# Kernel optimization log

Hardware: AMD Instinct MI355X
Metric: run time of the kernel (lower is better)

Reference implementation:

```python
import jax, jax.numpy as jnp
import numpy as np

N_NODES = 50000
N_EDGES = 800000
IN_FEATS = 128
HIDDEN = 128
NUM_CLASSES = 47


def setup_inputs() -> dict:
    key = jax.random.key(0)
    k1, k2, k3, k4 = jax.random.split(key, 4)
    features = jax.random.normal(k1, (N_NODES, IN_FEATS), dtype=jnp.float32)
    edge_index = jax.random.randint(k2, (2, N_EDGES), 0, N_NODES, dtype=jnp.int32)
    # Glorot-style init for weights, zeros for bias (DGL GraphConv defaults)
    W1 = jax.random.normal(k3, (IN_FEATS, HIDDEN), dtype=jnp.float32) * (1.0 / np.sqrt(IN_FEATS))
    b1 = jnp.zeros((HIDDEN,), dtype=jnp.float32)
    W2 = jax.random.normal(k4, (HIDDEN, NUM_CLASSES), dtype=jnp.float32) * (1.0 / np.sqrt(HIDDEN))
    b2 = jnp.zeros((NUM_CLASSES,), dtype=jnp.float32)
    return {"features": features, "edge_index": edge_index,
            "W1": W1, "b1": b1, "W2": W2, "b2": b2}


def _graph_conv(x, W, b, src, dst, norm_src, norm_dst, n_nodes):
    # DGL GraphConv, norm='both': D_dst^{-1/2} A D_src^{-1/2} (X W) + b
    h = (x * norm_src[:, None]) @ W            # transform before aggregation
    agg = jax.ops.segment_sum(h[src], dst, num_segments=n_nodes)
    return agg * norm_dst[:, None] + b


def reference(features, edge_index, W1, b1, W2, b2):
    src, dst = edge_index[0], edge_index[1]
    n = features.shape[0]
    ones = jnp.ones((src.shape[0],), dtype=features.dtype)
    deg_out = jax.ops.segment_sum(ones, src, num_segments=n)
    deg_in = jax.ops.segment_sum(ones, dst, num_segments=n)
    norm_src = jax.lax.rsqrt(jnp.clip(deg_out, 1.0))   # d_out^{-1/2}, clamp >= 1
    norm_dst = jax.lax.rsqrt(jnp.clip(deg_in, 1.0))    # d_in^{-1/2}, clamp >= 1

    h = _graph_conv(features, W1, b1, src, dst, norm_src, norm_dst, n)
    h = jax.nn.relu(h)
    out = _graph_conv(h, W2, b2, src, dst, norm_src, norm_dst, n)
    return out
```

## Files before the change

kernel.cpp:

```cpp
#include <hip/hip_runtime.h>
#include <hip/hip_fp16.h>

#define N_NODES 50000
#define N_EDGES 800000
#define IN_F 128
#define HID 128
#define NCLS 47
#define H2S 48
#define W2C 64
#define NCH 196
#define TM 32
#define XTS 40
#define NB 128
#define CHUNK 6250
#define NDW 25000

struct __align__(8)  h2x2 { __half2 a, b; };
struct __align__(16) h2x4 { __half2 a, b, c, d; };

__global__ __launch_bounds__(256) void hist_kernel(const int* __restrict__ ei,
                                                   unsigned int* __restrict__ Pdst,
                                                   unsigned int* __restrict__ Psrc) {
    __shared__ unsigned int h[NDW];
    const bool is_src = blockIdx.x >= NB;
    const int b = is_src ? blockIdx.x - NB : blockIdx.x;
    const int* ids = is_src ? ei : ei + N_EDGES;
    for (int j = threadIdx.x; j < NDW; j += 256) h[j] = 0u;
    __syncthreads();
    const int e0 = b * CHUNK;
    for (int k = threadIdx.x; k < CHUNK; k += 256) {
        int v = ids[e0 + k];
        atomicAdd(&h[v >> 1], (v & 1) ? (1u << 16) : 1u);
    }
    __syncthreads();
    unsigned int* P = (is_src ? Psrc : Pdst) + (size_t)b * NDW;
    for (int j = threadIdx.x; j < NDW; j += 256) P[j] = h[j];
}

__global__ __launch_bounds__(256) void reduce_kernel(unsigned int* __restrict__ Pdst,
                                                     const unsigned int* __restrict__ Psrc,
                                                     int* __restrict__ cnt_in,
                                                     float* __restrict__ norm_src,
                                                     float* __restrict__ norm_dst,
                                                     int* __restrict__ chunk_sums) {
    __shared__ int sm[256];
    const int t = threadIdx.x;
    const int j = blockIdx.x * 256 + t;
    unsigned int al = 0, ah = 0;
    if (j < NDW) {
        for (int b = 0; b < NB; ++b) {
            unsigned int v = Pdst[(size_t)b * NDW + j];
            Pdst[(size_t)b * NDW + j] = al | (ah << 16);
            al += v & 0xffffu;
            ah += v >> 16;
        }
        cnt_in[2 * j] = (int)al;
        cnt_in[2 * j + 1] = (int)ah;
        norm_dst[2 * j]     = rsqrtf(fmaxf((float)al, 1.0f));
        norm_dst[2 * j + 1] = rsqrtf(fmaxf((float)ah, 1.0f));
        unsigned int sl = 0, sh = 0;
        for (int b = 0; b < NB; ++b) {
            unsigned int v = Psrc[(size_t)b * NDW + j];
            sl += v & 0xffffu;
            sh += v >> 16;
        }
        norm_src[2 * j]     = rsqrtf(fmaxf((float)sl, 1.0f));
        norm_src[2 * j + 1] = rsqrtf(fmaxf((float)sh, 1.0f));
    }
    sm[t] = (j < NDW) ? (int)(al + ah) : 0;
    __syncthreads();
    const int hh = t & 127;
    for (int off = 64; off > 0; off >>= 1) {
        if (hh < off) sm[t] += sm[t + off];
        __syncthreads();
    }
    if (hh == 0) chunk_sums[2 * blockIdx.x + (t >> 7)] = sm[t];
}

__global__ __launch_bounds__(256) void scan2_pad_kernel(const int* __restrict__ chunk_sums,
                                                        int* __restrict__ chunk_base,
                                                        const float* __restrict__ W2,
                                                        float* __restrict__ W2p) {
    __shared__ int sm[256];
    int t = threadIdx.x;
    int v = (t < NCH) ? chunk_sums[t] : 0;
    sm[t] = v;
    __syncthreads();
    for (int off = 1; off < 256; off <<= 1) {
        int u = (t >= off) ? sm[t - off] : 0;
        __syncthreads();
        sm[t] += u;
        __syncthreads();
    }
    if (t < NCH) chunk_base[t] = sm[t] - v;
    for (int idx = t; idx < HID * W2C; idx += 256) {
        int k = idx >> 6, c = idx & 63;
        W2p[idx] = (c < NCLS) ? W2[k * NCLS + c] : 0.f;
    }
}

__global__ __launch_bounds__(256) void scan3_kernel(const int* __restrict__ cnt_in,
                                                    const int* __restrict__ chunk_base,
                                                    int* __restrict__ offsets) {
    __shared__ int sm[256];
    int t = threadIdx.x;
    int idx = blockIdx.x * 256 + t;
    int v = (idx < N_NODES) ? cnt_in[idx] : 0;
    sm[t] = v;
    __syncthreads();
    for (int off = 1; off < 256; off <<= 1) {
        int u = (t >= off) ? sm[t - off] : 0;
        __syncthreads();
        sm[t] += u;
        __syncthreads();
    }
    if (idx < N_NODES) offsets[idx] = chunk_base[blockIdx.x] + sm[t] - v;
    if (blockIdx.x == 0 && t == 0) offsets[N_NODES] = N_EDGES;
}

__global__ __launch_bounds__(256) void fill_kernel(const int* __restrict__ src,
                                                   const int* __restrict__ dst,
                                                   const int* __restrict__ offsets,
                                                   const unsigned int* __restrict__ Pdst,
                                                   int* __restrict__ csr_src) {
    __shared__ unsigned int cur[NDW];
    const int b = blockIdx.x;
    for (int j = threadIdx.x; j < NDW; j += 256) cur[j] = 0u;
    __syncthreads();
    const unsigned int* base = Pdst + (size_t)b * NDW;
    const int e0 = b * CHUNK;
    for (int k = threadIdx.x; k < CHUNK; k += 256) {
        int d = dst[e0 + k];
        unsigned int old = atomicAdd(&cur[d >> 1], (d & 1) ? (1u << 16) : 1u);
        unsigned int rank = (d & 1) ? (old >> 16) : (old & 0xffffu);
        unsigned int pb = base[d >> 1];
        unsigned int bh = (d & 1) ? (pb >> 16) : (pb & 0xffffu);
        csr_src[offsets[d] + (int)bh + (int)rank] = src[e0 + k];
    }
}

__global__ __launch_bounds__(128) void gemm1_kernel(const float* __restrict__ X,
                                                    const float* __restrict__ W1,
                                                    const float* __restrict__ norm_src,
                                                    __half* __restrict__ H1h) {
    __shared__ __align__(16) float xs[IN_F * XTS];
    const int t = threadIdx.x;
    const int row0 = blockIdx.x * TM;
#pragma unroll
    for (int i = 0; i < 8; ++i) {
        int id = t + 128 * i;
        int r = id & 31;
        int q = id >> 5;
        int row = row0 + r;
        float4 v = make_float4(0.f, 0.f, 0.f, 0.f);
        float ns = 0.f;
        if (row < N_NODES) {
            v = *(const float4*)&X[(size_t)row * IN_F + 4 * q];
            ns = norm_src[row];
        }
        xs[(4 * q + 0) * XTS + r] = v.x * ns;
        xs[(4 * q + 1) * XTS + r] = v.y * ns;
        xs[(4 * q + 2) * XTS + r] = v.z * ns;
        xs[(4 * q + 3) * XTS + r] = v.w * ns;
    }
    __syncthreads();
    const int c = t & 31;
    const int rg = t >> 5;
    float accA[4][4] = {{0.f}};
    float accB[4][4] = {{0.f}};
#pragma unroll 4
    for (int k = 0; k < IN_F; ++k) {
        const float4 w4 = *(const float4*)&W1[k * HID + 4 * c];
        const float4 a4 = *(const float4*)&xs[k * XTS + 4 * rg];
        const float4 b4 = *(const float4*)&xs[k * XTS + 16 + 4 * rg];
        const float wv[4] = {w4.x, w4.y, w4.z, w4.w};
        const float av[4] = {a4.x, a4.y, a4.z, a4.w};
        const float bv[4] = {b4.x, b4.y, b4.z, b4.w};
#pragma unroll
        for (int i = 0; i < 4; ++i)
#pragma unroll
            for (int j = 0; j < 4; ++j) {
                accA[i][j] += av[i] * wv[j];
                accB[i][j] += bv[i] * wv[j];
            }
    }
#pragma unroll
    for (int i = 0; i < 4; ++i) {
        int rowA = row0 + 4 * rg + i;
        int rowB = rowA + 16;
        if (rowA < N_NODES) {
            h2x2 p = {__floats2half2_rn(accA[i][0], accA[i][1]),
                      __floats2half2_rn(accA[i][2], accA[i][3])};
            *(h2x2*)&H1h[(size_t)rowA * HID + 4 * c] = p;
        }
        if (rowB < N_NODES) {
            h2x2 p = {__floats2half2_rn(accB[i][0], accB[i][1]),
                      __floats2half2_rn(accB[i][2], accB[i][3])};
            *(h2x2*)&H1h[(size_t)rowB * HID + 4 * c] = p;
        }
    }
}

__global__ __launch_bounds__(256) void gather1_kernel(const __half* __restrict__ H1h,
        const int* __restrict__ offsets, const int* __restrict__ csr_src,
        const float* __restrict__ b1, const float* __restrict__ norm_src,
        const float* __restrict__ norm_dst, __half* __restrict__ Hrelu16) {
    const int lane = threadIdx.x & 63;
    const int half = lane >> 5;
    const int fl = lane & 31;
    const int row = blockIdx.x * 4 + (threadIdx.x >> 6);
    const int beg = offsets[row], end = offsets[row + 1];
    float a0 = 0.f, a1 = 0.f, a2 = 0.f, a3 = 0.f;
    for (int base = beg; base < end; base += 64) {
        int idx = 0;
        if (base + lane < end) idx = csr_src[base + lane];
        const int cnt = min(end - base, 64);
        int j = 0;
        for (; j + 8 <= cnt; j += 8) {
            int s0 = __shfl(idx, j + half);
            int s1 = __shfl(idx, j + 2 + half);
            int s2 = __shfl(idx, j + 4 + half);
            int s3 = __shfl(idx, j + 6 + half);
            h2x2 v0 = *(const h2x2*)&H1h[(size_t)s0 * HID + 4 * fl];
            h2x2 v1 = *(const h2x2*)&H1h[(size_t)s1 * HID + 4 * fl];
            h2x2 v2 = *(const h2x2*)&H1h[(size_t)s2 * HID + 4 * fl];
            h2x2 v3 = *(const h2x2*)&H1h[(size_t)s3 * HID + 4 * fl];
            float2 p0 = __half22float2(v0.a), q0 = __half22float2(v0.b);
            float2 p1 = __half22float2(v1.a), q1 = __half22float2(v1.b);
            float2 p2 = __half22float2(v2.a), q2 = __half22float2(v2.b);
            float2 p3 = __half22float2(v3.a), q3 = __half22float2(v3.b);
            a0 += (p0.x + p1.x) + (p2.x + p3.x);
            a1 += (p0.y + p1.y) + (p2.y + p3.y);
            a2 += (q0.x + q1.x) + (q2.x + q3.x);
            a3 += (q0.y + q1.y) + (q2.y + q3.y);
        }
        for (; j + 2 <= cnt; j += 2) {
            int s = __shfl(idx, j + half);
            h2x2 v = *(const h2x2*)&H1h[(size_t)s * HID + 4 * fl];
            float2 p = __half22float2(v.a), q = __half22float2(v.b);
            a0 += p.x; a1 += p.y; a2 += q.x; a3 += q.y;
        }
        if (j < cnt) {
            int s = __shfl(idx, j);
            if (half == 0) {
                h2x2 v = *(const h2x2*)&H1h[(size_t)s * HID + 4 * fl];
                float2 p = __half22float2(v.a), q = __half22float2(v.b);
                a0 += p.x; a1 += p.y; a2 += q.x; a3 += q.y;
            }
        }
    }
    a0 += __shfl_xor(a0, 32);
    a1 += __shfl_xor(a1, 32);
    a2 += __shfl_xor(a2, 32);
    a3 += __shfl_xor(a3, 32);
    if (half == 0) {
        float nd = norm_dst[row], ns = norm_src[row];
        float4 bb = *(const float4*)&b1[4 * fl];
        float v0 = fmaxf(a0 * nd + bb.x, 0.f) * ns;
        float v1 = fmaxf(a1 * nd + bb.y, 0.f) * ns;
        float v2 = fmaxf(a2 * nd + bb.z, 0.f) * ns;
        float v3 = fmaxf(a3 * nd + bb.w, 0.f) * ns;
        h2x2 p = {__floats2half2_rn(v0, v1), __floats2half2_rn(v2, v3)};
        *(h2x2*)&Hrelu16[(size_t)row * HID + 4 * fl] = p;
    }
}

__global__ __launch_bounds__(128) void gemm2_kernel(const __half* __restrict__ Hrelu16,
                                                    const float* __restrict__ W2p,
                                                    __half* __restrict__ H2h) {
    __shared__ __align__(16) float xs[HID * XTS];
    const int t = threadIdx.x;
    const int row0 = blockIdx.x * TM;
#pragma unroll
    for (int i = 0; i < 4; ++i) {
        int id = t + 128 * i;
        int r = id & 31;
        int g = id >> 5;
        int row = row0 + r;
        h2x4 v{};
        if (row < N_NODES) v = *(const h2x4*)&Hrelu16[(size_t)row * HID + 8 * g];
        float2 f0 = __half22float2(v.a), f1 = __half22float2(v.b);
        float2 f2 = __half22float2(v.c), f3 = __half22float2(v.d);
        xs[(8 * g + 0) * XTS + r] = f0.x;
        xs[(8 * g + 1) * XTS + r] = f0.y;
        xs[(8 * g + 2) * XTS + r] = f1.x;
        xs[(8 * g + 3) * XTS + r] = f1.y;
        xs[(8 * g + 4) * XTS + r] = f2.x;
        xs[(8 * g + 5) * XTS + r] = f2.y;
        xs[(8 * g + 6) * XTS + r] = f3.x;
        xs[(8 * g + 7) * XTS + r] = f3.y;
    }
    __syncthreads();
    const int c = t & 15;
    const int rg = t >> 4;
    float acc[4][4] = {{0.f}};
#pragma unroll 4
    for (int k = 0; k < HID; ++k) {
        const float4 w4 = *(const float4*)&W2p[k * W2C + 4 * c];
        const float4 a4 = *(const float4*)&xs[k * XTS + 4 * rg];
        const float wv[4] = {w4.x, w4.y, w4.z, w4.w};
        const float av[4] = {a4.x, a4.y, a4.z, a4.w};
#pragma unroll
        for (int i = 0; i < 4; ++i)
#pragma unroll
            for (int j = 0; j < 4; ++j)
                acc[i][j] += av[i] * wv[j];
    }
    if (c < 12) {
#pragma unroll
        for (int i = 0; i < 4; ++i) {
            int row = row0 + 4 * rg + i;
            if (row < N_NODES) {
                h2x2 p = {__floats2half2_rn(acc[i][0], acc[i][1]),
                          __floats2half2_rn(acc[i][2], acc[i][3])};
                *(h2x2*)&H2h[(size_t)row * H2S + 4 * c] = p;
            }
        }
    }
}

__global__ __launch_bounds__(256) void gather2_kernel(const __half* __restrict__ H2h,
        const int* __restrict__ offsets, const int* __restrict__ csr_src,
        const float* __restrict__ b2, const float* __restrict__ norm_dst,
        float* __restrict__ out) {
    const int lane = threadIdx.x & 63;
    const int row = blockIdx.x * 4 + (threadIdx.x >> 6);
    const int beg = offsets[row], end = offsets[row + 1];
    float acc = 0.f;
    for (int base = beg; base < end; base += 64) {
        int idx = 0;
        if (base + lane < end) idx = csr_src[base + lane];
        const int cnt = min(end - base, 64);
        int j = 0;
        for (; j + 4 <= cnt; j += 4) {
            int s0 = __shfl(idx, j), s1 = __shfl(idx, j + 1);
            int s2 = __shfl(idx, j + 2), s3 = __shfl(idx, j + 3);
            if (lane < H2S) {
                float f0 = __half2float(H2h[(size_t)s0 * H2S + lane]);
                float f1 = __half2float(H2h[(size_t)s1 * H2S + lane]);
                float f2 = __half2float(H2h[(size_t)s2 * H2S + lane]);
                float f3 = __half2float(H2h[(size_t)s3 * H2S + lane]);
                acc += (f0 + f1) + (f2 + f3);
            }
        }
        for (; j < cnt; ++j) {
            int s = __shfl(idx, j);
            if (lane < H2S) acc += __half2float(H2h[(size_t)s * H2S + lane]);
        }
    }
    if (lane < NCLS) out[(size_t)row * NCLS + lane] = acc * norm_dst[row] + b2[lane];
}

extern "C" void kernel_launch(void* const* d_in, const int* in_sizes, int n_in,
                              void* d_out, int out_size, void* d_ws, size_t ws_size,
                              hipStream_t stream) {
    const float* X  = (const float*)d_in[0];
    const int*   ei = (const int*)d_in[1];
    const float* W1 = (const float*)d_in[2];
    const float* b1 = (const float*)d_in[3];
    const float* W2 = (const float*)d_in[4];
    const float* b2 = (const float*)d_in[5];
    float* out = (float*)d_out;

    const int* src = ei;
    const int* dst = ei + N_EDGES;

    char* w = (char*)d_ws;
    auto alloc = [&](size_t bytes) {
        char* p = w;
        w += (bytes + 255) & ~(size_t)255;
        return p;
    };
    float*  norm_src   = (float*)alloc(N_NODES * 4);
    float*  norm_dst   = (float*)alloc(N_NODES * 4);
    int*    cnt_in     = (int*)alloc(N_NODES * 4);
    int*    offsets    = (int*)alloc((N_NODES + 1) * 4);
    int*    csr_src    = (int*)alloc((size_t)N_EDGES * 4);
    int*    chunk_sums = (int*)alloc(NCH * 4);
    int*    chunk_base = (int*)alloc(NCH * 4);
    float*  W2p        = (float*)alloc((size_t)HID * W2C * 4);
    __half* H1h        = (__half*)alloc((size_t)N_NODES * HID * 2);
    __half* Hrelu16    = (__half*)alloc((size_t)N_NODES * HID * 2);
    __half* H2h        = (__half*)alloc((size_t)N_NODES * H2S * 2);
    unsigned int* Pdst = (unsigned int*)alloc((size_t)NB * NDW * 4);
    unsigned int* Psrc = (unsigned int*)alloc((size_t)NB * NDW * 4);

    hist_kernel<<<2 * NB, 256, 0, stream>>>(ei, Pdst, Psrc);
    reduce_kernel<<<(NDW + 255) / 256, 256, 0, stream>>>(Pdst, Psrc, cnt_in,
                                                         norm_src, norm_dst, chunk_sums);
    scan2_pad_kernel<<<1, 256, 0, stream>>>(chunk_sums, chunk_base, W2, W2p);
    scan3_kernel<<<NCH, 256, 0, stream>>>(cnt_in, chunk_base, offsets);
    fill_kernel<<<NB, 256, 0, stream>>>(src, dst, offsets, Pdst, csr_src);

    gemm1_kernel<<<(N_NODES + TM - 1) / TM, 128, 0, stream>>>(X, W1, norm_src, H1h);
    gather1_kernel<<<N_NODES / 4, 256, 0, stream>>>(H1h, offsets, csr_src, b1,
                                                    norm_src, norm_dst, Hrelu16);
    gemm2_kernel<<<(N_NODES + TM - 1) / TM, 128, 0, stream>>>(Hrelu16, W2p, H2h);
    gather2_kernel<<<N_NODES / 4, 256, 0, stream>>>(H2h, offsets, csr_src, b2,
                                                    norm_dst, out);
}
```

Before: 252.9 us.

## Fuse histogram and first GEMM into one launch, move src norm into gather

The histogram blocks and the first-layer GEMM blocks now run in a single heterogeneous kernel. The GEMM no longer depends on norm_src, because the source-degree normalization is applied per edge inside gather1 via an extra norm_src load and shuffle. The histogram is split into two passes over half-sized LDS so the fused kernel's shared memory stays smaller. The two scan kernels are merged by having each block redo the tiny chunk-sum scan, which removes one launch. The tradeoffs are extra per-edge loads and FMAs in the gather, and a double pass over edges in the histogram.

Measured after the change: 249.0 us. About the same (-1.5%).

```diff
diff --git a/kernel.cpp b/kernel.cpp
--- a/kernel.cpp
+++ b/kernel.cpp
@@ -14,27 +14,83 @@
 #define NB 128
 #define CHUNK 6250
 #define NDW 25000
+#define HDW 12500
+#define MEGA_LDS 50176
 
 struct __align__(8)  h2x2 { __half2 a, b; };
 struct __align__(16) h2x4 { __half2 a, b, c, d; };
 
-__global__ __launch_bounds__(256) void hist_kernel(const int* __restrict__ ei,
-                                                   unsigned int* __restrict__ Pdst,
-                                                   unsigned int* __restrict__ Psrc) {
-    __shared__ unsigned int h[NDW];
-    const bool is_src = blockIdx.x >= NB;
-    const int b = is_src ? blockIdx.x - NB : blockIdx.x;
-    const int* ids = is_src ? ei : ei + N_EDGES;
-    for (int j = threadIdx.x; j < NDW; j += 256) h[j] = 0u;
-    __syncthreads();
-    const int e0 = b * CHUNK;
-    for (int k = threadIdx.x; k < CHUNK; k += 256) {
-        int v = ids[e0 + k];
-        atomicAdd(&h[v >> 1], (v & 1) ? (1u << 16) : 1u);
-    }
-    __syncthreads();
-    unsigned int* P = (is_src ? Psrc : Pdst) + (size_t)b * NDW;
-    for (int j = threadIdx.x; j < NDW; j += 256) P[j] = h[j];
+__global__ __launch_bounds__(256) void mega1_kernel(const int* __restrict__ ei,
+                                                    unsigned int* __restrict__ Pdst,
+                                                    unsigned int* __restrict__ Psrc,
+                                                    const float* __restrict__ X,
+                                                    const float* __restrict__ W1,
+                                                    __half* __restrict__ H1h) {
+    extern __shared__ __align__(16) char smem[];
+    const int t = threadIdx.x;
+    if (blockIdx.x < 2 * NB) {
+        unsigned int* h = (unsigned int*)smem;
+        const bool is_src = blockIdx.x >= NB;
+        const int b = is_src ? blockIdx.x - NB : blockIdx.x;
+        const int* ids = is_src ? ei : ei + N_EDGES;
+        unsigned int* P = (is_src ? Psrc : Pdst) + (size_t)b * NDW;
+        const int e0 = b * CHUNK;
+#pragma unroll
+        for (int p = 0; p < 2; ++p) {
+            for (int j = t; j < HDW; j += 256) h[j] = 0u;
+            __syncthreads();
+            for (int k = t; k < CHUNK; k += 256) {
+                int v = ids[e0 + k];
+                int rel = (v >> 1) - p * HDW;
+                if ((unsigned)rel < HDW)
+                    atomicAdd(&h[rel], (v & 1) ? (1u << 16) : 1u);
+            }
+            __syncthreads();
+            for (int j = t; j < HDW; j += 256) P[p * HDW + j] = h[j];
+            __syncthreads();
+        }
+    } else {
+        float* xs = (float*)smem;
+        const int row0 = (blockIdx.x - 2 * NB) * TM;
+#pragma unroll
+        for (int i = 0; i < 4; ++i) {
+            int id = t + 256 * i;
+            int r = id & 31;
+            int q = id >> 5;
+            int row = row0 + r;
+            float4 v = make_float4(0.f, 0.f, 0.f, 0.f);
+            if (row < N_NODES) v = *(const float4*)&X[(size_t)row * IN_F + 4 * q];
+            xs[(4 * q + 0) * XTS + r] = v.x;
+            xs[(4 * q + 1) * XTS + r] = v.y;
+            xs[(4 * q + 2) * XTS + r] = v.z;
+            xs[(4 * q + 3) * XTS + r] = v.w;
+        }
+        __syncthreads();
+        const int c = t & 31;
+        const int rg = t >> 5;
+        float acc[4][4] = {{0.f}};
+#pragma unroll 4
+        for (int k = 0; k < IN_F; ++k) {
+            const float4 w4 = *(const float4*)&W1[k * HID + 4 * c];
+            const float4 a4 = *(const float4*)&xs[k * XTS + 4 * rg];
+            const float wv[4] = {w4.x, w4.y, w4.z, w4.w};
+            const float av[4] = {a4.x, a4.y, a4.z, a4.w};
+#pragma unroll
+            for (int i = 0; i < 4; ++i)
+#pragma unroll
+                for (int j = 0; j < 4; ++j)
+                    acc[i][j] += av[i] * wv[j];
+        }
+#pragma unroll
+        for (int i = 0; i < 4; ++i) {
+            int row = row0 + 4 * rg + i;
+            if (row < N_NODES) {
+                h2x2 p = {__floats2half2_rn(acc[i][0], acc[i][1]),
+                          __floats2half2_rn(acc[i][2], acc[i][3])};
+                *(h2x2*)&H1h[(size_t)row * HID + 4 * c] = p;
+            }
+        }
+    }
 }
 
 __global__ __launch_bounds__(256) void reduce_kernel(unsigned int* __restrict__ Pdst,
@@ -77,12 +133,13 @@
     if (hh == 0) chunk_sums[2 * blockIdx.x + (t >> 7)] = sm[t];
 }
 
-__global__ __launch_bounds__(256) void scan2_pad_kernel(const int* __restrict__ chunk_sums,
-                                                        int* __restrict__ chunk_base,
-                                                        const float* __restrict__ W2,
-                                                        float* __restrict__ W2p) {
+__global__ __launch_bounds__(256) void scan3_kernel(const int* __restrict__ cnt_in,
+                                                    const int* __restrict__ chunk_sums,
+                                                    int* __restrict__ offsets,
+                                                    const float* __restrict__ W2,
+                                                    float* __restrict__ W2p) {
     __shared__ int sm[256];
-    int t = threadIdx.x;
+    const int t = threadIdx.x;
     int v = (t < NCH) ? chunk_sums[t] : 0;
     sm[t] = v;
     __syncthreads();
@@ -92,21 +149,11 @@
         sm[t] += u;
         __syncthreads();
     }
-    if (t < NCH) chunk_base[t] = sm[t] - v;
-    for (int idx = t; idx < HID * W2C; idx += 256) {
-        int k = idx >> 6, c = idx & 63;
-        W2p[idx] = (c < NCLS) ? W2[k * NCLS + c] : 0.f;
-    }
-}
-
-__global__ __launch_bounds__(256) void scan3_kernel(const int* __restrict__ cnt_in,
-                                                    const int* __restrict__ chunk_base,
-                                                    int* __restrict__ offsets) {
-    __shared__ int sm[256];
-    int t = threadIdx.x;
-    int idx = blockIdx.x * 256 + t;
-    int v = (idx < N_NODES) ? cnt_in[idx] : 0;
-    sm[t] = v;
+    const int basev = (blockIdx.x == 0) ? 0 : sm[blockIdx.x - 1];
+    __syncthreads();
+    const int idx = blockIdx.x * 256 + t;
+    int c = (idx < N_NODES) ? cnt_in[idx] : 0;
+    sm[t] = c;
     __syncthreads();
     for (int off = 1; off < 256; off <<= 1) {
         int u = (t >= off) ? sm[t - off] : 0;
@@ -114,8 +161,14 @@
         sm[t] += u;
         __syncthreads();
     }
-    if (idx < N_NODES) offsets[idx] = chunk_base[blockIdx.x] + sm[t] - v;
-    if (blockIdx.x == 0 && t == 0) offsets[N_NODES] = N_EDGES;
+    if (idx < N_NODES) offsets[idx] = basev + sm[t] - c;
+    if (blockIdx.x == 0) {
+        if (t == 0) offsets[N_NODES] = N_EDGES;
+        for (int i2 = t; i2 < HID * W2C; i2 += 256) {
+            int k = i2 >> 6, cc = i2 & 63;
+            W2p[i2] = (cc < NCLS) ? W2[k * NCLS + cc] : 0.f;
+        }
+    }
 }
 
 __global__ __launch_bounds__(256) void fill_kernel(const int* __restrict__ src,
@@ -136,68 +189,6 @@
         unsigned int pb = base[d >> 1];
         unsigned int bh = (d & 1) ? (pb >> 16) : (pb & 0xffffu);
         csr_src[offsets[d] + (int)bh + (int)rank] = src[e0 + k];
-    }
-}
-
-__global__ __launch_bounds__(128) void gemm1_kernel(const float* __restrict__ X,
-                                                    const float* __restrict__ W1,
-                                                    const float* __restrict__ norm_src,
-                                                    __half* __restrict__ H1h) {
-    __shared__ __align__(16) float xs[IN_F * XTS];
-    const int t = threadIdx.x;
-    const int row0 = blockIdx.x * TM;
-#pragma unroll
-    for (int i = 0; i < 8; ++i) {
-        int id = t + 128 * i;
-        int r = id & 31;
-        int q = id >> 5;
-        int row = row0 + r;
-        float4 v = make_float4(0.f, 0.f, 0.f, 0.f);
-        float ns = 0.f;
-        if (row < N_NODES) {
-            v = *(const float4*)&X[(size_t)row * IN_F + 4 * q];
-            ns = norm_src[row];
-        }
-        xs[(4 * q + 0) * XTS + r] = v.x * ns;
-        xs[(4 * q + 1) * XTS + r] = v.y * ns;
-        xs[(4 * q + 2) * XTS + r] = v.z * ns;
-        xs[(4 * q + 3) * XTS + r] = v.w * ns;
-    }
-    __syncthreads();
-    const int c = t & 31;
-    const int rg = t >> 5;
-    float accA[4][4] = {{0.f}};
-    float accB[4][4] = {{0.f}};
-#pragma unroll 4
-    for (int k = 0; k < IN_F; ++k) {
-        const float4 w4 = *(const float4*)&W1[k * HID + 4 * c];
-        const float4 a4 = *(const float4*)&xs[k * XTS + 4 * rg];
-        const float4 b4 = *(const float4*)&xs[k * XTS + 16 + 4 * rg];
-        const float wv[4] = {w4.x, w4.y, w4.z, w4.w};
-        const float av[4] = {a4.x, a4.y, a4.z, a4.w};
-        const float bv[4] = {b4.x, b4.y, b4.z, b4.w};
-#pragma unroll
-        for (int i = 0; i < 4; ++i)
-#pragma unroll
-            for (int j = 0; j < 4; ++j) {
-                accA[i][j] += av[i] * wv[j];
-                accB[i][j] += bv[i] * wv[j];
-            }
-    }
-#pragma unroll
-    for (int i = 0; i < 4; ++i) {
-        int rowA = row0 + 4 * rg + i;
-        int rowB = rowA + 16;
-        if (rowA < N_NODES) {
-            h2x2 p = {__floats2half2_rn(accA[i][0], accA[i][1]),
-                      __floats2half2_rn(accA[i][2], accA[i][3])};
-            *(h2x2*)&H1h[(size_t)rowA * HID + 4 * c] = p;
-        }
-        if (rowB < N_NODES) {
-            h2x2 p = {__floats2half2_rn(accB[i][0], accB[i][1]),
-                      __floats2half2_rn(accB[i][2], accB[i][3])};
-            *(h2x2*)&H1h[(size_t)rowB * HID + 4 * c] = p;
-        }
     }
 }
 
@@ -213,14 +204,18 @@
     float a0 = 0.f, a1 = 0.f, a2 = 0.f, a3 = 0.f;
     for (int base = beg; base < end; base += 64) {
         int idx = 0;
-        if (base + lane < end) idx = csr_src[base + lane];
+        float nsv = 0.f;
+        if (base + lane < end) {
+            idx = csr_src[base + lane];
+            nsv = norm_src[idx];
+        }
         const int cnt = min(end - base, 64);
         int j = 0;
         for (; j + 8 <= cnt; j += 8) {
-            int s0 = __shfl(idx, j + half);
-            int s1 = __shfl(idx, j + 2 + half);
-            int s2 = __shfl(idx, j + 4 + half);
-            int s3 = __shfl(idx, j + 6 + half);
+            int s0 = __shfl(idx, j + half);      float n0 = __shfl(nsv, j + half);
+            int s1 = __shfl(idx, j + 2 + half);  float n1 = __shfl(nsv, j + 2 + half);
+            int s2 = __shfl(idx, j + 4 + half);  float n2 = __shfl(nsv, j + 4 + half);
+            int s3 = __shfl(idx, j + 6 + half);  float n3 = __shfl(nsv, j + 6 + half);
             h2x2 v0 = *(const h2x2*)&H1h[(size_t)s0 * HID + 4 * fl];
             h2x2 v1 = *(const h2x2*)&H1h[(size_t)s1 * HID + 4 * fl];
             h2x2 v2 = *(const h2x2*)&H1h[(size_t)s2 * HID + 4 * fl];
@@ -229,23 +224,31 @@
             float2 p1 = __half22float2(v1.a), q1 = __half22float2(v1.b);
             float2 p2 = __half22float2(v2.a), q2 = __half22float2(v2.b);
             float2 p3 = __half22float2(v3.a), q3 = __half22float2(v3.b);
-            a0 += (p0.x + p1.x) + (p2.x + p3.x);
-            a1 += (p0.y + p1.y) + (p2.y + p3.y);
-            a2 += (q0.x + q1.x) + (q2.x + q3.x);
-            a3 += (q0.y + q1.y) + (q2.y + q3.y);
+            a0 = fmaf(p0.x, n0, a0); a1 = fmaf(p0.y, n0, a1);
+            a2 = fmaf(q0.x, n0, a2); a3 = fmaf(q0.y, n0, a3);
+            a0 = fmaf(p1.x, n1, a0); a1 = fmaf(p1.y, n1, a1);
+            a2 = fmaf(q1.x, n1, a2); a3 = fmaf(q1.y, n1, a3);
+            a0 = fmaf(p2.x, n2, a0); a1 = fmaf(p2.y, n2, a1);
+            a2 = fmaf(q2.x, n2, a2); a3 = fmaf(q2.y, n2, a3);
+            a0 = fmaf(p3.x, n3, a0); a1 = fmaf(p3.y, n3, a1);
+            a2 = fmaf(q3.x, n3, a2); a3 = fmaf(q3.y, n3, a3);
         }
         for (; j + 2 <= cnt; j += 2) {
             int s = __shfl(idx, j + half);
+            float n = __shfl(nsv, j + half);
             h2x2 v = *(const h2x2*)&H1h[(size_t)s * HID + 4 * fl];
             float2 p = __half22float2(v.a), q = __half22float2(v.b);
-            a0 += p.x; a1 += p.y; a2 += q.x; a3 += q.y;
+            a0 = fmaf(p.x, n, a0); a1 = fmaf(p.y, n, a1);
+            a2 = fmaf(q.x, n, a2); a3 = fmaf(q.y, n, a3);
         }
         if (j < cnt) {
             int s = __shfl(idx, j);
+            float n = __shfl(nsv, j);
             if (half == 0) {
                 h2x2 v = *(const h2x2*)&H1h[(size_t)s * HID + 4 * fl];
                 float2 p = __half22float2(v.a), q = __half22float2(v.b);
-                a0 += p.x; a1 += p.y; a2 += q.x; a3 += q.y;
+                a0 = fmaf(p.x, n, a0); a1 = fmaf(p.y, n, a1);
+                a2 = fmaf(q.x, n, a2); a3 = fmaf(q.y, n, a3);
             }
         }
     }
@@ -256,10 +259,10 @@
     if (half == 0) {
         float nd = norm_dst[row], ns = norm_src[row];
         float4 bb = *(const float4*)&b1[4 * fl];
-        float v0 = fmaxf(a0 * nd + bb.x, 0.f) * ns;
-        float v1 = fmaxf(a1 * nd + bb.y, 0.f) * ns;
-        float v2 = fmaxf(a2 * nd + bb.z, 0.f) * ns;
-        float v3 = fmaxf(a3 * nd + bb.w, 0.f) * ns;
+        float v0 = fmaxf(fmaf(a0, nd, bb.x), 0.f) * ns;
+        float v1 = fmaxf(fmaf(a1, nd, bb.y), 0.f) * ns;
+        float v2 = fmaxf(fmaf(a2, nd, bb.z), 0.f) * ns;
+        float v3 = fmaxf(fmaf(a3, nd, bb.w), 0.f) * ns;
         h2x2 p = {__floats2half2_rn(v0, v1), __floats2half2_rn(v2, v3)};
         *(h2x2*)&Hrelu16[(size_t)row * HID + 4 * fl] = p;
     }
@@ -377,7 +380,6 @@
     int*    offsets    = (int*)alloc((N_NODES + 1) * 4);
     int*    csr_src    = (int*)alloc((size_t)N_EDGES * 4);
     int*    chunk_sums = (int*)alloc(NCH * 4);
-    int*    chunk_base = (int*)alloc(NCH * 4);
     float*  W2p        = (float*)alloc((size_t)HID * W2C * 4);
     __half* H1h        = (__half*)alloc((size_t)N_NODES * HID * 2);
     __half* Hrelu16    = (__half*)alloc((size_t)N_NODES * HID * 2);
@@ -385,17 +387,17 @@
     unsigned int* Pdst = (unsigned int*)alloc((size_t)NB * NDW * 4);
     unsigned int* Psrc = (unsigned int*)alloc((size_t)NB * NDW * 4);
 
-    hist_kernel<<<2 * NB, 256, 0, stream>>>(ei, Pdst, Psrc);
+    const int gemm_blocks = (N_NODES + TM - 1) / TM;
+    mega1_kernel<<<2 * NB + gemm_blocks, 256, MEGA_LDS, stream>>>(ei, Pdst, Psrc,
+                                                                  X, W1, H1h);
     reduce_kernel<<<(NDW + 255) / 256, 256, 0, stream>>>(Pdst, Psrc, cnt_in,
                                                          norm_src, norm_dst, chunk_sums);
-    scan2_pad_kernel<<<1, 256, 0, stream>>>(chunk_sums, chunk_base, W2, W2p);
-    scan3_kernel<<<NCH, 256, 0, stream>>>(cnt_in, chunk_base, offsets);
+    scan3_kernel<<<NCH, 256, 0, stream>>>(cnt_in, chunk_sums, offsets, W2, W2p);
     fill_kernel<<<NB, 256, 0, stream>>>(src, dst, offsets, Pdst, csr_src);
 
-    gemm1_kernel<<<(N_NODES + TM - 1) / TM, 128, 0, stream>>>(X, W1, norm_src, H1h);
     gather1_kernel<<<N_NODES / 4, 256, 0, stream>>>(H1h, offsets, csr_src, b1,
                                                     norm_src, norm_dst, Hrelu16);
-    gemm2_kernel<<<(N_NODES + TM - 1) / TM, 128, 0, stream>>>(Hrelu16, W2p, H2h);
+    gemm2_kernel<<<gemm_blocks, 128, 0, stream>>>(Hrelu16, W2p, H2h);
     gather2_kernel<<<N_NODES / 4, 256, 0, stream>>>(H2h, offsets, csr_src, b2,
                                                     norm_dst, out);
 }
```
